# Performance work log

Hardware: AMD Instinct MI355X
Metric: run time of the kernel (lower is better)

## Reference

```python
import jax, jax.numpy as jnp
import numpy as np

B, F, P, H = 8192, 32, 512, 256
EPS_W = 1e-8   # weight-normalization eps from _normalize_weights
EPS_LN = 1e-5  # torch LayerNorm default eps


def setup_inputs() -> dict:
    key = jax.random.key(0)
    k0, k1, k2, k3, k4 = jax.random.split(key, 5)
    phys = jax.random.normal(k0, (B, F, P), dtype=jnp.float32)
    ratios = jax.random.uniform(k1, (B, F), dtype=jnp.float32)
    lengths = jax.random.randint(k2, (B,), 1, F + 1, dtype=jnp.int32)
    ln_gamma = jnp.ones((P,), jnp.float32)
    ln_beta = jnp.zeros((P,), jnp.float32)
    lim1 = float(np.sqrt(6.0 / (P + H)))  # xavier_uniform
    W1 = jax.random.uniform(k3, (H, P), jnp.float32, -lim1, lim1)
    b1 = jnp.zeros((H,), jnp.float32)
    lim2 = float(np.sqrt(6.0 / (H + 1)))
    W2 = jax.random.uniform(k4, (1, H), jnp.float32, -lim2, lim2)
    b2 = jnp.zeros((1,), jnp.float32)
    return dict(phys=phys, ratios=ratios, lengths=lengths,
                ln_gamma=ln_gamma, ln_beta=ln_beta,
                W1=W1, b1=b1, W2=W2, b2=b2)


def reference(phys, ratios, lengths, ln_gamma, ln_beta, W1, b1, W2, b2):
    # Ragged weighted mix: mask padded fragments, normalize weights per sample.
    mask = (jnp.arange(F)[None, :] < lengths[:, None]).astype(phys.dtype)  # [B,F]
    w = ratios * mask
    w = w / (jnp.sum(w, axis=-1, keepdims=True) + EPS_W)
    mix = jnp.einsum('bf,bfp->bp', w, phys)  # [B,P]
    # Head: LayerNorm(P) -> Linear(P,H) -> ReLU -> Linear(H,1)
    mu = jnp.mean(mix, axis=-1, keepdims=True)
    var = jnp.mean((mix - mu) ** 2, axis=-1, keepdims=True)
    xn = (mix - mu) * jax.lax.rsqrt(var + EPS_LN) * ln_gamma + ln_beta
    h = jax.nn.relu(xn @ W1.T + b1)  # [B,H]
    y = h @ W2.T + b2                # [B,1]
    return jnp.nan_to_num(y)
```

## Files before the change

kernel.cpp:

```cpp
#include <hip/hip_runtime.h>
#include <math.h>

#define BB 8192
#define FF 32
#define PP 512
#define HH 256
#define S  8

__global__ void transpose_w1(const float* __restrict__ W1, float* __restrict__ W1T) {
    int p = blockIdx.x;
    int j = threadIdx.x;
    W1T[((p >> 2) * HH + j) * 4 + (p & 3)] = W1[j * PP + p];
}

__global__ __launch_bounds__(256, 4)
void fused_physchem(const float* __restrict__ phys,
                    const float* __restrict__ ratios,
                    const int*   __restrict__ lengths,
                    const float* __restrict__ gamma,
                    const float* __restrict__ beta,
                    const float* __restrict__ W1T,
                    const float* __restrict__ b1,
                    const float* __restrict__ W2,
                    const float* __restrict__ b2,
                    float* __restrict__ out) {
    constexpr int PADP = PP + 4;
    __shared__ float wts[S][FF];
    __shared__ int   slen[S];
    __shared__ __align__(16) float xn[S][PADP];
    __shared__ float red[4][4][2];
    __shared__ float redy[4][S];

    const int tid  = threadIdx.x;
    const int wave = tid >> 6;
    const int lane = tid & 63;
    const int b0   = blockIdx.x * S;

    {
        int s = tid >> 5;
        int f = tid & 31;
        int len = lengths[b0 + s];
        float r = ratios[(b0 + s) * FF + f];
        float w = (f < len) ? r : 0.0f;
        float sum = w;
        #pragma unroll
        for (int m = 16; m >= 1; m >>= 1) sum += __shfl_xor(sum, m, 32);
        wts[s][f] = w / (sum + 1e-8f);
        if (f == 0) slen[s] = len;
    }
    __syncthreads();

    const int pt = tid & 127;
    const int sh = tid >> 7;
    float4 mixacc[4];
    {
        const float4* phys4 = (const float4*)phys;
        #pragma unroll
        for (int k = 0; k < 4; ++k) {
            const int s   = 2 * k + sh;
            const int len = slen[s];
            const float4* row = phys4 + (size_t)(b0 + s) * FF * (PP / 4) + pt;
            float4 a = make_float4(0.f, 0.f, 0.f, 0.f);
            #pragma unroll 8
            for (int f = 0; f < len; ++f) {
                float  w = wts[s][f];
                float4 v = row[(size_t)f * (PP / 4)];
                a.x += w * v.x; a.y += w * v.y;
                a.z += w * v.z; a.w += w * v.w;
            }
            mixacc[k] = a;
        }
    }

    #pragma unroll
    for (int k = 0; k < 4; ++k) {
        float4 a = mixacc[k];
        float sum = a.x + a.y + a.z + a.w;
        float sq  = a.x * a.x + a.y * a.y + a.z * a.z + a.w * a.w;
        #pragma unroll
        for (int m = 32; m >= 1; m >>= 1) {
            sum += __shfl_xor(sum, m, 64);
            sq  += __shfl_xor(sq,  m, 64);
        }
        if (lane == 0) { red[wave][k][0] = sum; red[wave][k][1] = sq; }
    }
    __syncthreads();
    {
        float4 g  = ((const float4*)gamma)[pt];
        float4 be = ((const float4*)beta)[pt];
        const int wbase = sh * 2;
        #pragma unroll
        for (int k = 0; k < 4; ++k) {
            const int s = 2 * k + sh;
            float sum = red[wbase][k][0] + red[wbase + 1][k][0];
            float sq  = red[wbase][k][1] + red[wbase + 1][k][1];
            float mu  = sum * (1.0f / PP);
            float var = sq * (1.0f / PP) - mu * mu;
            float inv = rsqrtf(var + 1e-5f);
            float4 a = mixacc[k];
            float4 o;
            o.x = (a.x - mu) * inv * g.x + be.x;
            o.y = (a.y - mu) * inv * g.y + be.y;
            o.z = (a.z - mu) * inv * g.z + be.z;
            o.w = (a.w - mu) * inv * g.w + be.w;
            *(float4*)&xn[s][4 * pt] = o;
        }
    }
    __syncthreads();

    float hacc[S];
    #pragma unroll
    for (int s = 0; s < S; ++s) hacc[s] = 0.f;
    {
        const int j = tid;
        for (int p0 = 0; p0 < PP; p0 += 4) {
            float4 wv = *(const float4*)&W1T[((p0 >> 2) * HH + j) * 4];
            #pragma unroll
            for (int s = 0; s < S; ++s) {
                float4 xv = *(const float4*)&xn[s][p0];
                hacc[s] += wv.x * xv.x + wv.y * xv.y + wv.z * xv.z + wv.w * xv.w;
            }
        }
    }
    float b1j = b1[tid];
    float w2j = W2[tid];
    #pragma unroll
    for (int s = 0; s < S; ++s) {
        float h = hacc[s] + b1j;
        h = h > 0.f ? h : 0.f;
        float v = h * w2j;
        #pragma unroll
        for (int m = 32; m >= 1; m >>= 1) v += __shfl_xor(v, m, 64);
        if (lane == 0) redy[wave][s] = v;
    }
    __syncthreads();
    if (tid < S) {
        int s = tid;
        float y = redy[0][s] + redy[1][s] + redy[2][s] + redy[3][s] + b2[0];
        if (isnan(y)) y = 0.f;
        else if (isinf(y)) y = (y > 0.f) ? 3.402823466e38f : -3.402823466e38f;
        out[b0 + s] = y;
    }
}

extern "C" void kernel_launch(void* const* d_in, const int* in_sizes, int n_in,
                              void* d_out, int out_size, void* d_ws, size_t ws_size,
                              hipStream_t stream) {
    const float* phys    = (const float*)d_in[0];
    const float* ratios  = (const float*)d_in[1];
    const int*   lengths = (const int*)  d_in[2];
    const float* gamma   = (const float*)d_in[3];
    const float* beta    = (const float*)d_in[4];
    const float* W1      = (const float*)d_in[5];
    const float* b1      = (const float*)d_in[6];
    const float* W2      = (const float*)d_in[7];
    const float* b2      = (const float*)d_in[8];
    float* out = (float*)d_out;
    float* W1T = (float*)d_ws;

    transpose_w1<<<dim3(PP), dim3(HH), 0, stream>>>(W1, W1T);
    fused_physchem<<<dim3(BB / S), dim3(256), 0, stream>>>(
        phys, ratios, lengths, gamma, beta, W1T, b1, W2, b2, out);
}
```

Before: 700.4 us.

## Process 16 samples per block and register-tile the W1 GEMV per wave

Doubles the samples handled per block from 8 to 16, halving the grid and the number of times W1T is streamed per sample. The hidden-layer product is restructured so each wave owns 4 samples and each lane computes 4 hidden units. Each W1T float4 is reused across 4 samples in registers, and the final reduction stays within one wave, which removes a shared-memory step and a block barrier. In exchange it uses more registers and LDS and halves the occupancy hint, which may weaken latency hiding on the memory-bound phys read.

```diff
diff --git a/kernel.cpp b/kernel.cpp
--- a/kernel.cpp
+++ b/kernel.cpp
@@ -5,7 +5,7 @@
 #define FF 32
 #define PP 512
 #define HH 256
-#define S  8
+#define S  16
 
 __global__ void transpose_w1(const float* __restrict__ W1, float* __restrict__ W1T) {
     int p = blockIdx.x;
@@ -13,7 +13,7 @@
     W1T[((p >> 2) * HH + j) * 4 + (p & 3)] = W1[j * PP + p];
 }
 
-__global__ __launch_bounds__(256, 4)
+__global__ __launch_bounds__(256, 2)
 void fused_physchem(const float* __restrict__ phys,
                     const float* __restrict__ ratios,
                     const int*   __restrict__ lengths,
@@ -28,8 +28,7 @@
     __shared__ float wts[S][FF];
     __shared__ int   slen[S];
     __shared__ __align__(16) float xn[S][PADP];
-    __shared__ float red[4][4][2];
-    __shared__ float redy[4][S];
+    __shared__ float red[4][8][2];
 
     const int tid  = threadIdx.x;
     const int wave = tid >> 6;
@@ -37,26 +36,30 @@
     const int b0   = blockIdx.x * S;
 
     {
-        int s = tid >> 5;
+        int g = tid >> 5;
         int f = tid & 31;
-        int len = lengths[b0 + s];
-        float r = ratios[(b0 + s) * FF + f];
-        float w = (f < len) ? r : 0.0f;
-        float sum = w;
         #pragma unroll
-        for (int m = 16; m >= 1; m >>= 1) sum += __shfl_xor(sum, m, 32);
-        wts[s][f] = w / (sum + 1e-8f);
-        if (f == 0) slen[s] = len;
+        for (int rep = 0; rep < 2; ++rep) {
+            int s = g + 8 * rep;
+            int len = lengths[b0 + s];
+            float r = ratios[(b0 + s) * FF + f];
+            float w = (f < len) ? r : 0.0f;
+            float sum = w;
+            #pragma unroll
+            for (int m = 16; m >= 1; m >>= 1) sum += __shfl_xor(sum, m, 32);
+            wts[s][f] = w / (sum + 1e-8f);
+            if (f == 0) slen[s] = len;
+        }
     }
     __syncthreads();
 
     const int pt = tid & 127;
     const int sh = tid >> 7;
-    float4 mixacc[4];
+    float4 mixacc[8];
     {
         const float4* phys4 = (const float4*)phys;
         #pragma unroll
-        for (int k = 0; k < 4; ++k) {
+        for (int k = 0; k < 8; ++k) {
             const int s   = 2 * k + sh;
             const int len = slen[s];
             const float4* row = phys4 + (size_t)(b0 + s) * FF * (PP / 4) + pt;
@@ -73,7 +76,7 @@
     }
 
     #pragma unroll
-    for (int k = 0; k < 4; ++k) {
+    for (int k = 0; k < 8; ++k) {
         float4 a = mixacc[k];
         float sum = a.x + a.y + a.z + a.w;
         float sq  = a.x * a.x + a.y * a.y + a.z * a.z + a.w * a.w;
@@ -90,7 +93,7 @@
         float4 be = ((const float4*)beta)[pt];
         const int wbase = sh * 2;
         #pragma unroll
-        for (int k = 0; k < 4; ++k) {
+        for (int k = 0; k < 8; ++k) {
             const int s = 2 * k + sh;
             float sum = red[wbase][k][0] + red[wbase + 1][k][0];
             float sq  = red[wbase][k][1] + red[wbase + 1][k][1];
@@ -108,38 +111,56 @@
     }
     __syncthreads();
 
-    float hacc[S];
+    float hacc[4][4];
     #pragma unroll
-    for (int s = 0; s < S; ++s) hacc[s] = 0.f;
+    for (int t = 0; t < 4; ++t)
+        #pragma unroll
+        for (int jj = 0; jj < 4; ++jj) hacc[t][jj] = 0.f;
     {
-        const int j = tid;
-        for (int p0 = 0; p0 < PP; p0 += 4) {
-            float4 wv = *(const float4*)&W1T[((p0 >> 2) * HH + j) * 4];
+        const int sb = wave * 4;
+        const float4* W1T4 = (const float4*)W1T;
+        for (int c = 0; c < PP / 4; ++c) {
+            float4 wv[4];
             #pragma unroll
-            for (int s = 0; s < S; ++s) {
-                float4 xv = *(const float4*)&xn[s][p0];
-                hacc[s] += wv.x * xv.x + wv.y * xv.y + wv.z * xv.z + wv.w * xv.w;
+            for (int jj = 0; jj < 4; ++jj)
+                wv[jj] = W1T4[c * HH + lane + 64 * jj];
+            #pragma unroll
+            for (int t = 0; t < 4; ++t) {
+                float4 xv = *(const float4*)&xn[sb + t][4 * c];
+                #pragma unroll
+                for (int jj = 0; jj < 4; ++jj)
+                    hacc[t][jj] += wv[jj].x * xv.x + wv[jj].y * xv.y
+                                 + wv[jj].z * xv.z + wv[jj].w * xv.w;
             }
         }
     }
-    float b1j = b1[tid];
-    float w2j = W2[tid];
-    #pragma unroll
-    for (int s = 0; s < S; ++s) {
-        float h = hacc[s] + b1j;
-        h = h > 0.f ? h : 0.f;
-        float v = h * w2j;
+    {
+        const int sb = wave * 4;
+        float b1v[4], w2v[4];
         #pragma unroll
-        for (int m = 32; m >= 1; m >>= 1) v += __shfl_xor(v, m, 64);
-        if (lane == 0) redy[wave][s] = v;
-    }
-    __syncthreads();
-    if (tid < S) {
-        int s = tid;
-        float y = redy[0][s] + redy[1][s] + redy[2][s] + redy[3][s] + b2[0];
-        if (isnan(y)) y = 0.f;
-        else if (isinf(y)) y = (y > 0.f) ? 3.402823466e38f : -3.402823466e38f;
-        out[b0 + s] = y;
+        for (int jj = 0; jj < 4; ++jj) {
+            b1v[jj] = b1[lane + 64 * jj];
+            w2v[jj] = W2[lane + 64 * jj];
+        }
+        float b2v = b2[0];
+        #pragma unroll
+        for (int t = 0; t < 4; ++t) {
+            float v = 0.f;
+            #pragma unroll
+            for (int jj = 0; jj < 4; ++jj) {
+                float h = hacc[t][jj] + b1v[jj];
+                h = h > 0.f ? h : 0.f;
+                v += h * w2v[jj];
+            }
+            #pragma unroll
+            for (int m = 32; m >= 1; m >>= 1) v += __shfl_xor(v, m, 64);
+            if (lane == 0) {
+                float y = v + b2v;
+                if (isnan(y)) y = 0.f;
+                else if (isinf(y)) y = (y > 0.f) ? 3.402823466e38f : -3.402823466e38f;
+                out[b0 + sb + t] = y;
+            }
+        }
     }
 }
 
```

After: 688.6 us. About the same (-1.7%).
